# Performance work log

Measured on AMD Instinct MI355X. Metric: run time of the kernel, lower is better.

The kernel has to match this reference:

```python
import jax, jax.numpy as jnp
import numpy as np

B, N, IN_F, E, H, A = 8, 1024, 1024, 256, 4, 64
ALPHA = 0.2          # leaky relu slope
NEG = -9e15          # mask value from original code


def setup_inputs() -> dict:
    key = jax.random.key(0)
    k = jax.random.split(key, 7)
    x = jax.random.normal(k[0], (B * N, IN_F), dtype=jnp.float32)
    adj = jax.random.randint(k[1], (B, N, N), 0, 2, dtype=jnp.int32)
    # per-head GAT params: W (H, IN_F, E); a split into a1, a2 (H, E) each,
    # since cat([Wh_i, Wh_j]) @ a == Wh_i @ a1 + Wh_j @ a2 exactly.
    W = jax.random.normal(k[2], (H, IN_F, E), dtype=jnp.float32) * 0.05
    a1 = jax.random.normal(k[3], (H, E), dtype=jnp.float32) * 0.05
    a2 = jax.random.normal(k[4], (H, E), dtype=jnp.float32) * 0.05
    W_act = jax.random.normal(k[5], (H * E, A), dtype=jnp.float32) * 0.05
    b_act = jnp.zeros((A,), dtype=jnp.float32)
    return {"x": x, "adj": adj, "W": W, "a1": a1, "a2": a2,
            "W_act": W_act, "b_act": b_act}


def reference(x, adj, W, a1, a2, W_act, b_act):
    b, n, _ = adj.shape
    xr = x.reshape(b, n, -1)                                   # (B, N, IN_F)
    Wh = jnp.einsum('bni,hio->hbno', xr, W)                    # (H, B, N, E)
    f1 = jnp.einsum('hbno,ho->hbn', Wh, a1)                    # a . Wh_i part
    f2 = jnp.einsum('hbno,ho->hbn', Wh, a2)                    # a . Wh_j part
    e = jax.nn.leaky_relu(f1[..., :, None] + f2[..., None, :], ALPHA)  # (H,B,N,N)
    e = jnp.where(adj[None] > 0, e, NEG)
    att = jax.nn.softmax(e, axis=-1)                           # masked softmax
    h_prime = jnp.einsum('hbnm,hbmo->hbno', att, Wh)           # (H, B, N, E)
    h_prime = jax.nn.elu(h_prime)                              # concat=True -> elu
    feat = jnp.transpose(h_prime, (1, 2, 0, 3)).reshape(b * n, H * E)
    return feat @ W_act + b_act                                # (B*N, A)
```

## Files before the change

kernel.cpp:

```cpp
#include <hip/hip_runtime.h>
#include <stdint.h>

typedef __attribute__((ext_vector_type(8))) short short8;
typedef __attribute__((ext_vector_type(4))) float f32x4;
typedef __attribute__((ext_vector_type(16))) float f32x16;


__device__ __forceinline__ float b2f(unsigned short u) {
    union { unsigned int i; float f; } v; v.i = ((unsigned int)u) << 16; return v.f;
}
__device__ __forceinline__ unsigned short f2b(float f) {
    union { float f; unsigned int i; } v; v.f = f;
    unsigned int u = v.i;
    u = (u + 0x7FFFu + ((u >> 16) & 1u)) >> 16;
    return (unsigned short)u;
}
__device__ __forceinline__ void glds16(const void* g, const void* l) {
    __builtin_amdgcn_global_load_lds(
        (const __attribute__((address_space(1))) unsigned int*)g,
        (__attribute__((address_space(3))) unsigned int*)l, 16, 0, 0);
}

__device__ __forceinline__ void cvt8(const void* in, unsigned short* out,
                                     int f, int grp) {
    if (f) {
        ((ushort4*)out)[grp * 2]     = ((const ushort4*)in)[grp * 2];
        ((ushort4*)out)[grp * 2 + 1] = ((const ushort4*)in)[grp * 2 + 1];
    } else {
        const float4* p = (const float4*)in + (size_t)grp * 2;
        float4 a = p[0], b = p[1];
        ushort4 o0, o1;
        o0.x = f2b(a.x); o0.y = f2b(a.y); o0.z = f2b(a.z); o0.w = f2b(a.w);
        o1.x = f2b(b.x); o1.y = f2b(b.y); o1.z = f2b(b.z); o1.w = f2b(b.w);
        ((ushort4*)out)[grp * 2]     = o0;
        ((ushort4*)out)[grp * 2 + 1] = o1;
    }
}

__global__ __launch_bounds__(256) void prep_all(
        const unsigned int* __restrict__ x4,
        const void* __restrict__ x, const void* __restrict__ W,
        const void* __restrict__ Wact,
        const void* __restrict__ a1, const void* __restrict__ a2,
        const void* __restrict__ bact,
        unsigned short* __restrict__ xb, unsigned short* __restrict__ WT,
        unsigned short* __restrict__ WactT,
        unsigned short* __restrict__ a1b, unsigned short* __restrict__ a2b,
        unsigned short* __restrict__ bactb,
        int* __restrict__ flag, float4* __restrict__ fz) {
    __shared__ unsigned int tile[64 * 65];
    __shared__ int sflag;
    int tid = threadIdx.x;
    int bid = blockIdx.x;
    if (bid >= 4352 && bid < 4416) {
        fz[(bid - 4352) * 256 + tid] = float4{0.f, 0.f, 0.f, 0.f};
        return;
    }
    if (tid < 64) {
        unsigned int wv = x4[tid];
        unsigned int e = (wv >> 7) & 0xFF;
        unsigned long long m = __ballot(e >= 100 && e <= 140);
        if (tid == 0) sflag = (__popcll(m) >= 48) ? 1 : 0;
    }
    __syncthreads();
    int f = sflag;

    if (bid < 4096) {
        cvt8(x, xb, f, bid * 256 + tid);
        return;
    }
    if (bid == 4416) {
        if (tid == 0) flag[0] = f;
        if (tid < 128) cvt8(a1, a1b, f, tid);
        else           cvt8(a2, a2b, f, tid - 128);
        if (tid < 8)   cvt8(bact, bactb, f, tid);
        return;
    }
    const void* in; unsigned short* out; int C, bt, c0, r0;
    if (bid < 4352) {
        int lb = bid - 4096;
        in = W; out = WT; C = 256;
        c0 = (lb & 3) * 64;
        r0 = ((lb >> 2) & 15) * 64;
        bt = lb >> 6;
    } else {
        int lb = bid - 4417;
        in = Wact; out = WactT; C = 64;
        c0 = 0; r0 = lb * 64; bt = 0;
    }
    int rl = tid >> 2;
    int cc = (tid & 3) * 16;
    size_t ibase = ((size_t)bt * 1024 + (r0 + rl)) * C + c0 + cc;
    unsigned short v[16];
    if (f) {
        const unsigned short* p = (const unsigned short*)in + ibase;
        short8 a = *(const short8*)p;
        short8 b = *(const short8*)(p + 8);
#pragma unroll
        for (int j = 0; j < 8; j++) { v[j] = (unsigned short)a[j]; v[8 + j] = (unsigned short)b[j]; }
    } else {
        const float* p = (const float*)in + ibase;
#pragma unroll
        for (int j = 0; j < 16; j++) v[j] = f2b(p[j]);
    }
#pragma unroll
    for (int j = 0; j < 16; j++)
        tile[(cc + j) * 65 + rl] = v[j];
    __syncthreads();
    int cl = tid >> 2;
    int rch = (tid & 3) * 16;
    unsigned short o[16];
#pragma unroll
    for (int j = 0; j < 16; j++)
        o[j] = (unsigned short)tile[cl * 65 + rch + j];
    unsigned short* op = out + ((size_t)bt * C + (c0 + cl)) * 1024 + r0 + rch;
#pragma unroll
    for (int q = 0; q < 4; q++) {
        ushort4 s; s.x = o[q*4]; s.y = o[q*4+1]; s.z = o[q*4+2]; s.w = o[q*4+3];
        ((ushort4*)op)[q] = s;
    }
}

__global__ void pack_adj(const int* __restrict__ adj,
                         unsigned int* __restrict__ maskT) {
    int gid = blockIdx.x * 256 + threadIdx.x;
    int lane = threadIdx.x & 63;
    unsigned long long m = __ballot(adj[gid] > 0);
    if (lane == 0) {
        int lin = gid >> 6;
        int mw = (lin & 15) * 2;
        int bn = lin >> 4;
        int b = bn >> 10, n = bn & 1023;
        maskT[(size_t)(b * 32 + mw) * 1024 + n]     = (unsigned int)m;
        maskT[(size_t)(b * 32 + mw + 1) * 1024 + n] = (unsigned int)(m >> 32);
    }
}

__global__ __launch_bounds__(256) void k1_gemm(
        const unsigned short* __restrict__ x,
        const unsigned short* __restrict__ WT,
        unsigned short* __restrict__ WhF,
        const unsigned short* __restrict__ a1b,
        const unsigned short* __restrict__ a2b,
        float* __restrict__ f1, float* __restrict__ f2) {
    __shared__ unsigned short smA[8 * 512];
    __shared__ unsigned short smB[8 * 512];
    int tid = threadIdx.x;
    int w = tid >> 6, lane = tid & 63;
    int lr = lane & 15, lq = lane >> 4;
    int col0 = blockIdx.x * 128;
    int row0 = blockIdx.y * 128;
    int h = col0 >> 8;
    int e_base = col0 & 255;
    int b = row0 >> 10;
    int m_base = row0 & 1023;
    int wr = w >> 1, wc = w & 1;

    f32x4 acc[4][4] = {};

    for (int k0 = 0; k0 < 1024; k0 += 32) {
        __syncthreads();
#pragma unroll
        for (int s = 0; s < 2; s++) {
            int g = 2 * w + s;
            const unsigned short* srcA =
                x + (size_t)(row0 + g * 16 + lr) * 1024 + k0 + lq * 8;
            glds16(srcA, &smA[g * 512]);
            const unsigned short* srcB =
                WT + (size_t)(h * 256 + e_base + g * 16 + lr) * 1024 + k0 + lq * 8;
            glds16(srcB, &smB[g * 512]);
        }
        __syncthreads();
        short8 af[4], bf[4];
#pragma unroll
        for (int i = 0; i < 4; i++)
            af[i] = *(const short8*)&smA[(wr * 4 + i) * 512 + lane * 8];
#pragma unroll
        for (int j = 0; j < 4; j++)
            bf[j] = *(const short8*)&smB[(wc * 4 + j) * 512 + lane * 8];
#pragma unroll
        for (int i = 0; i < 4; i++)
#pragma unroll
            for (int j = 0; j < 4; j++)
                acc[i][j] = __builtin_amdgcn_mfma_f32_16x16x32_bf16(
                    af[i], bf[j], acc[i][j], 0, 0, 0);
    }

    int hb = h * 8 + b;
#pragma unroll
    for (int i = 0; i < 4; i++) {
#pragma unroll
        for (int j = 0; j < 4; j++) {
            int e = e_base + (wc * 4 + j) * 16 + lr;
            int et = e >> 5, e31 = e & 31;
            int m16 = (m_base >> 4) + wr * 4 + i;
            ushort4 vs;
            vs.x = f2b(acc[i][j][0]);
            vs.y = f2b(acc[i][j][1]);
            vs.z = f2b(acc[i][j][2]);
            vs.w = f2b(acc[i][j][3]);
            size_t idx = ((size_t)((hb * 8 + et) * 64 + m16) * 512)
                         + ((lq >> 1) * 32 + e31) * 8 + (lq & 1) * 4;
            *(ushort4*)&WhF[idx] = vs;
        }
    }

    const float LOG2E = 1.44269504f;
    float a1v[4], a2v[4];
#pragma unroll
    for (int j = 0; j < 4; j++) {
        int e = e_base + (wc * 4 + j) * 16 + lr;
        a1v[j] = b2f(a1b[h * 256 + e]);
        a2v[j] = b2f(a2b[h * 256 + e]);
    }
#pragma unroll
    for (int i = 0; i < 4; i++) {
#pragma unroll
        for (int reg = 0; reg < 4; reg++) {
            float s1 = 0.f, s2 = 0.f;
#pragma unroll
            for (int j = 0; j < 4; j++) {
                s1 += acc[i][j][reg] * a1v[j];
                s2 += acc[i][j][reg] * a2v[j];
            }
            s1 += __shfl_xor(s1, 1, 64); s2 += __shfl_xor(s2, 1, 64);
            s1 += __shfl_xor(s1, 2, 64); s2 += __shfl_xor(s2, 2, 64);
            s1 += __shfl_xor(s1, 4, 64); s2 += __shfl_xor(s2, 4, 64);
            s1 += __shfl_xor(s1, 8, 64); s2 += __shfl_xor(s2, 8, 64);
            if (lr == 0) {
                int m = m_base + (wr * 4 + i) * 16 + lq * 4 + reg;
                atomicAdd(&f1[hb * 1024 + m], s1 * LOG2E);
                atomicAdd(&f2[hb * 1024 + m], s2 * LOG2E);
            }
        }
    }
}

__global__ __launch_bounds__(256, 2) void k2_attn(
        const unsigned short* __restrict__ WhF,
        const unsigned int* __restrict__ maskT,
        const float* __restrict__ f1, const float* __restrict__ f2,
        unsigned short* __restrict__ feat) {
    int tid = threadIdx.x;
    int w = tid >> 6, lane = tid & 63;
    int l5 = lane >> 5, l31 = lane & 31;
    int bid = blockIdx.x;
    int xcd = bid & 7, idx = bid >> 3;
    int hb = xcd + 8 * (idx >> 4);
    int sub = idx & 15;
    int wid = sub * 4 + w;
    int rg = wid >> 1;
    int ehalf = wid & 1;
    int n0 = rg * 32;
    int h = hb >> 3, b = hb & 7;
    int row = n0 + l31;
    float f1n = f1[hb * 1024 + row];
    const unsigned short* whb = WhF + (size_t)(hb * 8 + ehalf * 4) * 64 * 512
                                + lane * 8;
    const unsigned int* mrow = maskT + (size_t)b * 32 * 1024 + row;
    const float* f2row = f2 + hb * 1024;

    f32x16 acc[4] = {};
    float den = 0.f;

    short8 buf[2][4][2];
#pragma unroll
    for (int et = 0; et < 4; et++)
#pragma unroll
        for (int ks = 0; ks < 2; ks++)
            buf[0][et][ks] = *(const short8*)(whb + (size_t)(et * 64 + ks) * 512);

#pragma unroll 2
    for (int m0 = 0; m0 < 1024; m0 += 32) {
        int p = (m0 >> 5) & 1;
        if (m0 + 32 < 1024) {
            int m16n = (m0 >> 4) + 2;
#pragma unroll
            for (int et = 0; et < 4; et++)
#pragma unroll
                for (int ks = 0; ks < 2; ks++)
                    buf[p ^ 1][et][ks] =
                        *(const short8*)(whb + (size_t)(et * 64 + m16n + ks) * 512);
        }
        unsigned int mw = mrow[(size_t)(m0 >> 5) * 1024];
        float4 fA0 = *(const float4*)(f2row + m0 + l5 * 8);
        float4 fA1 = *(const float4*)(f2row + m0 + l5 * 8 + 4);
        float4 fB0 = *(const float4*)(f2row + m0 + 16 + l5 * 8);
        float4 fB1 = *(const float4*)(f2row + m0 + 16 + l5 * 8 + 4);
        float fm[16] = {fA0.x,fA0.y,fA0.z,fA0.w, fA1.x,fA1.y,fA1.z,fA1.w,
                        fB0.x,fB0.y,fB0.z,fB0.w, fB1.x,fB1.y,fB1.z,fB1.w};
        short8 af[2];
#pragma unroll
        for (int ks = 0; ks < 2; ks++) {
#pragma unroll
            for (int j = 0; j < 8; j++) {
                float t_ = f1n + fm[ks * 8 + j];
                float e_ = fmaxf(t_, 0.2f * t_);
                float pv = ((mw >> (ks * 16 + l5 * 8 + j)) & 1u) ? exp2f(e_) : 0.f;
                unsigned short pb = f2b(pv);
                af[ks][j] = (short)pb;
                den += b2f(pb);
            }
        }
#pragma unroll
        for (int et = 0; et < 4; et++)
#pragma unroll
            for (int ks = 0; ks < 2; ks++)
                acc[et] = __builtin_amdgcn_mfma_f32_32x32x16_bf16(
                    af[ks], buf[p][et][ks], acc[et], 0, 0, 0);
    }

    den += __shfl_xor(den, 32, 64);

#pragma unroll
    for (int reg = 0; reg < 16; reg++) {
        int r = (reg & 3) + 8 * (reg >> 2) + 4 * l5;
        float dr = __shfl(den, r, 64);
        float rdr = 1.0f / dr;
        int nn = n0 + r;
#pragma unroll
        for (int et = 0; et < 4; et++) {
            int e = ehalf * 128 + et * 32 + l31;
            float v = acc[et][reg] * rdr;
            float o = v > 0.f ? v : __expf(v) - 1.f;
            feat[(size_t)(b * 1024 + nn) * 1024 + h * 256 + e] = f2b(o);
        }
    }
}

__global__ __launch_bounds__(256) void k3_out(
        const unsigned short* __restrict__ feat,
        const unsigned short* __restrict__ WactT,
        const unsigned short* __restrict__ bact,
        void* __restrict__ out, const int* __restrict__ flag) {
    __shared__ unsigned short smA[2 * 512];
    __shared__ unsigned short smB[4 * 512];
    int tid = threadIdx.x;
    int w = tid >> 6, lane = tid & 63;
    int lr = lane & 15, lq = lane >> 4;
    int row0 = blockIdx.x * 32;
    int g = w & 1, ch = w >> 1;
    int bf16out = *flag;
    f32x4 acc[2] = {};

    for (int k0 = 0; k0 < 1024; k0 += 32) {
        __syncthreads();
        if (w < 2) {
            const unsigned short* src =
                feat + (size_t)(row0 + w * 16 + lr) * 1024 + k0 + lq * 8;
            glds16(src, &smA[w * 512]);
        } else {
#pragma unroll
            for (int s = 0; s < 2; s++) {
                int t = (w - 2) * 2 + s;
                const unsigned short* src =
                    WactT + (size_t)(t * 16 + lr) * 1024 + k0 + lq * 8;
                glds16(src, &smB[t * 512]);
            }
        }
        __syncthreads();
        short8 af = *(const short8*)&smA[g * 512 + lane * 8];
#pragma unroll
        for (int j = 0; j < 2; j++) {
            short8 bf = *(const short8*)&smB[(ch * 2 + j) * 512 + lane * 8];
            acc[j] = __builtin_amdgcn_mfma_f32_16x16x32_bf16(af, bf, acc[j], 0, 0, 0);
        }
    }
#pragma unroll
    for (int j = 0; j < 2; j++) {
        int col = ch * 32 + j * 16 + lr;
        float bv = b2f(bact[col]);
#pragma unroll
        for (int rr = 0; rr < 4; rr++) {
            int r = row0 + g * 16 + lq * 4 + rr;
            float val = acc[j][rr] + bv;
            if (bf16out) ((unsigned short*)out)[(size_t)r * 64 + col] = f2b(val);
            else         ((float*)out)[(size_t)r * 64 + col] = val;
        }
    }
}

extern "C" void kernel_launch(void* const* d_in, const int* in_sizes, int n_in,
                              void* d_out, int out_size, void* d_ws, size_t ws_size,
                              hipStream_t stream) {
    const void* x    = d_in[0];
    const int*  adj  = (const int*)d_in[1];
    const void* W    = d_in[2];
    const void* a1   = d_in[3];
    const void* a2   = d_in[4];
    const void* Wact = d_in[5];
    const void* bact = d_in[6];

    char* ws = (char*)d_ws;
    unsigned short* WhF   = (unsigned short*)(ws);
    unsigned short* xb    = (unsigned short*)(ws + 16777216);
    unsigned short* feat  = (unsigned short*)(ws + 16777216);
    unsigned short* WT    = (unsigned short*)(ws + 33554432);
    unsigned int*   maskT = (unsigned int*)(ws + 33554432);
    unsigned short* WactT = (unsigned short*)(ws + 35651584);
    float*          f1    = (float*)(ws + 35782656);
    float*          f2    = (float*)(ws + 35913728);
    unsigned short* a1b   = (unsigned short*)(ws + 36044800);
    unsigned short* a2b   = (unsigned short*)(ws + 36046848);
    unsigned short* bactb = (unsigned short*)(ws + 36048896);
    int*            flag  = (int*)(ws + 36049024);
    if (ws_size < (size_t)36049040) return;

    prep_all<<<4433, 256, 0, stream>>>((const unsigned int*)x, x, W, Wact,
                                       a1, a2, bact, xb, WT, WactT,
                                       a1b, a2b, bactb, flag, (float4*)f1);
    k1_gemm<<<dim3(8, 64), 256, 0, stream>>>(xb, WT, WhF, a1b, a2b, f1, f2);
    pack_adj<<<32768, 256, 0, stream>>>(adj, maskT);
    k2_attn<<<512, 256, 0, stream>>>(WhF, maskT, f1, f2, feat);
    k3_out<<<256, 256, 0, stream>>>(feat, WactT, bactb, d_out, flag);
}
```

Before: 226.3 us.

## Split attention probability computation across waves and share via LDS

The attention kernel now uses 512-thread blocks in which four waves split the 256-wide feature dimension of a 32-row group. Each wave computes only a quarter of the exp/mask probabilities, writes them to a shared LDS tile and reads back the full fragment after a barrier. This removes the duplicated exp work that each wave previously did, at the cost of a __syncthreads per iteration and a cross-wave denominator reduction. It also uses the packed bf16 convert instruction and prefetches the next mask word and f2 values one iteration ahead.

```diff
diff --git a/kernel.cpp b/kernel.cpp
--- a/kernel.cpp
+++ b/kernel.cpp
@@ -14,6 +14,17 @@
     unsigned int u = v.i;
     u = (u + 0x7FFFu + ((u >> 16) & 1u)) >> 16;
     return (unsigned short)u;
+}
+__device__ __forceinline__ unsigned int cvtpk(float a, float b) {
+    unsigned int r;
+    asm("v_cvt_pk_bf16_f32 %0, %1, %2" : "=v"(r) : "v"(a), "v"(b));
+    return r;
+}
+__device__ __forceinline__ float blo(unsigned int u) {
+    union { unsigned int i; float f; } v; v.i = u << 16; return v.f;
+}
+__device__ __forceinline__ float bhi(unsigned int u) {
+    union { unsigned int i; float f; } v; v.i = u & 0xFFFF0000u; return v.f;
 }
 __device__ __forceinline__ void glds16(const void* g, const void* l) {
     __builtin_amdgcn_global_load_lds(
@@ -236,91 +247,103 @@
     }
 }
 
-__global__ __launch_bounds__(256, 2) void k2_attn(
+__global__ __launch_bounds__(512, 4) void k2_attn(
         const unsigned short* __restrict__ WhF,
         const unsigned int* __restrict__ maskT,
         const float* __restrict__ f1, const float* __restrict__ f2,
         unsigned short* __restrict__ feat) {
+    __shared__ unsigned short ptile[2][2][32][40];
+    __shared__ float dred[2][4][32];
     int tid = threadIdx.x;
     int w = tid >> 6, lane = tid & 63;
+    int q = w & 3, wrg = w >> 2;
     int l5 = lane >> 5, l31 = lane & 31;
     int bid = blockIdx.x;
     int xcd = bid & 7, idx = bid >> 3;
     int hb = xcd + 8 * (idx >> 4);
-    int sub = idx & 15;
-    int wid = sub * 4 + w;
-    int rg = wid >> 1;
-    int ehalf = wid & 1;
-    int n0 = rg * 32;
+    int rgb = idx & 15;
+    int n0 = rgb * 64 + wrg * 32;
     int h = hb >> 3, b = hb & 7;
     int row = n0 + l31;
     float f1n = f1[hb * 1024 + row];
-    const unsigned short* whb = WhF + (size_t)(hb * 8 + ehalf * 4) * 64 * 512
+    const unsigned short* whb = WhF + (size_t)(hb * 8 + q * 2) * 64 * 512
                                 + lane * 8;
     const unsigned int* mrow = maskT + (size_t)b * 32 * 1024 + row;
-    const float* f2row = f2 + hb * 1024;
-
-    f32x16 acc[4] = {};
+    const float* f2p = f2 + hb * 1024 + q * 8 + l5 * 4;
+    int cshift = q * 8 + l5 * 4;
+
+    f32x16 acc[2] = {};
     float den = 0.f;
 
-    short8 buf[2][4][2];
-#pragma unroll
-    for (int et = 0; et < 4; et++)
+    short8 buf[2][2][2];
+#pragma unroll
+    for (int et = 0; et < 2; et++)
 #pragma unroll
         for (int ks = 0; ks < 2; ks++)
             buf[0][et][ks] = *(const short8*)(whb + (size_t)(et * 64 + ks) * 512);
 
+    unsigned int mw = mrow[0];
+    float4 fv = *(const float4*)f2p;
+
 #pragma unroll 2
     for (int m0 = 0; m0 < 1024; m0 += 32) {
-        int p = (m0 >> 5) & 1;
+        int cur = (m0 >> 5) & 1;
+        float fvv[4] = {fv.x, fv.y, fv.z, fv.w};
+        unsigned int mloc = mw >> cshift;
+        float pv[4];
+#pragma unroll
+        for (int j = 0; j < 4; j++) {
+            float t_ = f1n + fvv[j];
+            float e_ = fmaxf(t_, 0.2f * t_);
+            pv[j] = ((mloc >> j) & 1u) ? exp2f(e_) : 0.f;
+        }
+        unsigned int r0 = cvtpk(pv[0], pv[1]);
+        unsigned int r1 = cvtpk(pv[2], pv[3]);
+        den += (blo(r0) + bhi(r0)) + (blo(r1) + bhi(r1));
+        uint2 pr; pr.x = r0; pr.y = r1;
+        *(uint2*)&ptile[cur][wrg][l31][cshift] = pr;
+        unsigned int mwN = 0u; float4 fvN = fv;
+        if (m0 + 32 < 1024) {
+            mwN = mrow[(size_t)((m0 >> 5) + 1) * 1024];
+            fvN = *(const float4*)(f2p + m0 + 32);
+        }
+        __syncthreads();
+        short8 af0 = *(const short8*)&ptile[cur][wrg][l31][l5 * 8];
+        short8 af1 = *(const short8*)&ptile[cur][wrg][l31][16 + l5 * 8];
         if (m0 + 32 < 1024) {
             int m16n = (m0 >> 4) + 2;
 #pragma unroll
-            for (int et = 0; et < 4; et++)
+            for (int et = 0; et < 2; et++)
 #pragma unroll
                 for (int ks = 0; ks < 2; ks++)
-                    buf[p ^ 1][et][ks] =
+                    buf[cur ^ 1][et][ks] =
                         *(const short8*)(whb + (size_t)(et * 64 + m16n + ks) * 512);
         }
-        unsigned int mw = mrow[(size_t)(m0 >> 5) * 1024];
-        float4 fA0 = *(const float4*)(f2row + m0 + l5 * 8);
-        float4 fA1 = *(const float4*)(f2row + m0 + l5 * 8 + 4);
-        float4 fB0 = *(const float4*)(f2row + m0 + 16 + l5 * 8);
-        float4 fB1 = *(const float4*)(f2row + m0 + 16 + l5 * 8 + 4);
-        float fm[16] = {fA0.x,fA0.y,fA0.z,fA0.w, fA1.x,fA1.y,fA1.z,fA1.w,
-                        fB0.x,fB0.y,fB0.z,fB0.w, fB1.x,fB1.y,fB1.z,fB1.w};
-        short8 af[2];
-#pragma unroll
-        for (int ks = 0; ks < 2; ks++) {
-#pragma unroll
-            for (int j = 0; j < 8; j++) {
-                float t_ = f1n + fm[ks * 8 + j];
-                float e_ = fmaxf(t_, 0.2f * t_);
-                float pv = ((mw >> (ks * 16 + l5 * 8 + j)) & 1u) ? exp2f(e_) : 0.f;
-                unsigned short pb = f2b(pv);
-                af[ks][j] = (short)pb;
-                den += b2f(pb);
-            }
-        }
-#pragma unroll
-        for (int et = 0; et < 4; et++)
-#pragma unroll
-            for (int ks = 0; ks < 2; ks++)
-                acc[et] = __builtin_amdgcn_mfma_f32_32x32x16_bf16(
-                    af[ks], buf[p][et][ks], acc[et], 0, 0, 0);
+#pragma unroll
+        for (int et = 0; et < 2; et++) {
+            acc[et] = __builtin_amdgcn_mfma_f32_32x32x16_bf16(
+                af0, buf[cur][et][0], acc[et], 0, 0, 0);
+            acc[et] = __builtin_amdgcn_mfma_f32_32x32x16_bf16(
+                af1, buf[cur][et][1], acc[et], 0, 0, 0);
+        }
+        mw = mwN; fv = fvN;
     }
 
     den += __shfl_xor(den, 32, 64);
+    if (l5 == 0) dred[wrg][q][l31] = den;
+    __syncthreads();
+    float denf = dred[wrg][0][l31] + dred[wrg][1][l31]
+               + dred[wrg][2][l31] + dred[wrg][3][l31];
 
 #pragma unroll
     for (int reg = 0; reg < 16; reg++) {
         int r = (reg & 3) + 8 * (reg >> 2) + 4 * l5;
-        float dr = __shfl(den, r, 64);
+        float dr = __shfl(denf, r, 64);
         float rdr = 1.0f / dr;
         int nn = n0 + r;
 #pragma unroll
-        for (int et = 0; et < 4; et++) {
-            int e = ehalf * 128 + et * 32 + l31;
+        for (int et = 0; et < 2; et++) {
+            int e = q * 64 + et * 32 + l31;
             float v = acc[et][reg] * rdr;
             float o = v > 0.f ? v : __expf(v) - 1.f;
             feat[(size_t)(b * 1024 + nn) * 1024 + h * 256 + e] = f2b(o);
@@ -411,6 +434,6 @@
                                        a1b, a2b, bactb, flag, (float4*)f1);
     k1_gemm<<<dim3(8, 64), 256, 0, stream>>>(xb, WT, WhF, a1b, a2b, f1, f2);
     pack_adj<<<32768, 256, 0, stream>>>(adj, maskT);
-    k2_attn<<<512, 256, 0, stream>>>(WhF, maskT, f1, f2, feat);
+    k2_attn<<<512, 512, 0, stream>>>(WhF, maskT, f1, f2, feat);
     k3_out<<<256, 256, 0, stream>>>(feat, WactT, bactb, d_out, flag);
 }
```

Measured after the change: 208.4 us. -7.9%, faster.
